# Optimization experiments

Hardware: AMD Instinct MI355X
Metric: run time of the kernel (lower is better)

Reference implementation:

```python
import jax, jax.numpy as jnp
import numpy as np
from jax import lax

T = 32768
DUNITS = 1024
ATT_DIM = 512
EPROJS = 512
ACONV_CHANS = 32
ACONV_FILTS = 15  # kernel = 2*15+1 = 31


def setup_inputs() -> dict:
    key = jax.random.key(0)
    ks = jax.random.split(key, 8)
    dec_z = jax.random.normal(ks[0], (1, DUNITS), jnp.float32)
    att_prev = jax.random.uniform(ks[1], (1, T), jnp.float32)
    att_prev = att_prev / jnp.sum(att_prev, axis=1, keepdims=True)  # prob-like alignment
    pre_compute_enc_h = jax.random.normal(ks[2], (1, T, ATT_DIM), jnp.float32) * 0.1
    enc_h = jax.random.normal(ks[3], (1, T, EPROJS), jnp.float32)
    mask = jnp.zeros((1, T), jnp.float32)  # additive mask (0 = keep)
    conv_w = jax.random.normal(ks[4], (ACONV_CHANS, 1, 2 * ACONV_FILTS + 1), jnp.float32) * 0.1
    conv_b = jnp.zeros((ACONV_CHANS,), jnp.float32)
    W_att = jax.random.normal(ks[5], (ATT_DIM, ACONV_CHANS), jnp.float32) * 0.1
    W_dec = jax.random.normal(ks[6], (ATT_DIM, DUNITS), jnp.float32) * 0.03
    W_g = jax.random.normal(ks[7], (1, ATT_DIM), jnp.float32) * 0.05
    b_g = jnp.zeros((1,), jnp.float32)
    return {"dec_z": dec_z, "att_prev": att_prev, "pre_compute_enc_h": pre_compute_enc_h,
            "enc_h": enc_h, "mask": mask, "conv_w": conv_w, "conv_b": conv_b,
            "W_att": W_att, "W_dec": W_dec, "W_g": W_g, "b_g": b_g}


def reference(dec_z, att_prev, pre_compute_enc_h, enc_h, mask, conv_w, conv_b, W_att, W_dec, W_g, b_g):
    scaling = 2.0
    # location conv: att_prev [1,T] -> [1,C,T] (Conv2d with height-1 kernel == Conv1d)
    att_conv = lax.conv_general_dilated(
        att_prev[:, None, :], conv_w, window_strides=(1,),
        padding=[(ACONV_FILTS, ACONV_FILTS)],
        dimension_numbers=("NCH", "OIH", "NCH"))
    att_conv = att_conv + conv_b[None, :, None]          # [1,C,T]
    att_conv = jnp.einsum("bct,ac->bta", att_conv, W_att)  # mlp_att -> [1,T,att_dim]
    dec_z_tiled = (dec_z @ W_dec.T)[:, None, :]           # [1,1,att_dim]
    # gvec over tanh sum -> energies [1,T]
    e = jnp.einsum("bta,a->bt", jnp.tanh(pre_compute_enc_h + dec_z_tiled + att_conv), W_g[0]) + b_g[0]
    e = e + mask
    w = jax.nn.softmax(scaling * e, axis=1)               # [1,T]
    # forward-attention recurrence: shift-add-mul, then L1 normalize
    att_prev_shift = jnp.pad(att_prev, ((0, 0), (1, 0)))[:, :-1]
    w = (att_prev + att_prev_shift) * w
    w = jnp.clip(w, 1e-6, None)
    w = w / jnp.sum(w, axis=1, keepdims=True)             # L1 normalize (w > 0)
    c = jnp.sum(enc_h * w[:, :, None], axis=1)            # [1,eprojs]
    return (c, w)
```

## Files before the change

### kernel.cpp

```cpp
#include <hip/hip_runtime.h>

#define T_LEN 32768
#define ADIM  512
#define NDEC  1024
#define KTAPS 31

#define WS_BASE 0
#define WS_G    512
#define WS_SARR 16384
#define WS_BMAX 49152
#define WS_BSUM 49664
#define WS_SSUM 50176
#define WS_U    50432
#define WS_CREP 83968

__device__ __forceinline__ float fast_tanh(float x) {
    float e = __expf(2.0f * x);
    return 1.0f - 2.0f * __builtin_amdgcn_rcpf(e + 1.0f);
}

__device__ __forceinline__ float uniform_f(float v) {
    return __uint_as_float(__builtin_amdgcn_readfirstlane(__float_as_uint(v)));
}

__global__ __launch_bounds__(256) void k0_prep(
        const float* __restrict__ dec_z, const float* __restrict__ conv_w,
        const float* __restrict__ conv_b, const float* __restrict__ W_att,
        const float* __restrict__ W_dec, float* __restrict__ ws) {
    int b = blockIdx.x, tid = threadIdx.x;
    int lane = tid & 63, wave = tid >> 6;
    if (b < 64) {
        for (int s = 0; s < 2; ++s) {
            int a = b * 8 + wave * 2 + s;
            float sum = 0.f;
            #pragma unroll
            for (int i = 0; i < 16; ++i)
                sum += W_dec[a * NDEC + i * 64 + lane] * dec_z[i * 64 + lane];
            #pragma unroll
            for (int off = 32; off > 0; off >>= 1) sum += __shfl_xor(sum, off);
            if (lane == 0) {
                float bias = 0.f;
                #pragma unroll
                for (int c = 0; c < 32; ++c) bias += conv_b[c] * W_att[a * 32 + c];
                ws[WS_BASE + a] = sum + bias;
            }
        }
    } else if (b < 64 + KTAPS) {
        int k = b - 64;
        for (int r = 0; r < 2; ++r) {
            int a = tid + r * 256;
            float g = 0.f;
            #pragma unroll
            for (int c = 0; c < 32; ++c) g += conv_w[c * KTAPS + k] * W_att[a * 32 + c];
            ws[WS_G + k * ADIM + a] = g;
        }
    } else {
        if (tid == 0) ws[WS_SSUM] = 0.f;
    }
}

__global__ __launch_bounds__(512, 4) void k1_energy(
        const float* __restrict__ att_prev, const float* __restrict__ pre,
        const float* __restrict__ mask, const float* __restrict__ W_g,
        const float* __restrict__ b_g, float* __restrict__ ws) {
    __shared__ float Gs[KTAPS * ADIM];
    __shared__ float ap_s[96];
    __shared__ float wm[8], wz[8];
    int tid = threadIdx.x, lane = tid & 63, wave = tid >> 6;
    int t0 = blockIdx.x * 64;

    if (blockIdx.x < 32) ws[WS_CREP + blockIdx.x * 512 + tid] = 0.f;

    const float4* Gsrc = (const float4*)(ws + WS_G);
    float4* Gdst = (float4*)Gs;
    #pragma unroll
    for (int i = 0; i < 8; ++i) {
        int idx = tid + i * 512;
        if (idx < 3968) Gdst[idx] = Gsrc[idx];
    }
    if (tid < 94) {
        int g = t0 - 15 + tid;
        ap_s[tid] = (g >= 0 && g < T_LEN) ? att_prev[g] : 0.f;
    }
    __syncthreads();

    float bg = b_g[0];
    int tb_local = wave * 8;
    int tb = t0 + tb_local;

    float ap_u[38];
    #pragma unroll
    for (int i = 0; i < 38; ++i) ap_u[i] = uniform_f(ap_s[tb_local + i]);

    float ps[8];
    #pragma unroll
    for (int j = 0; j < 8; ++j) ps[j] = 0.f;

    #pragma unroll 1
    for (int half = 0; half < 2; ++half) {
        int aa = half * 256 + 4 * lane;
        float4 base = *(const float4*)(ws + WS_BASE + aa);
        float4 wg   = *(const float4*)(W_g + aa);

        float4 p[8];
        #pragma unroll
        for (int j = 0; j < 8; ++j)
            p[j] = *(const float4*)(pre + (size_t)(tb + j) * ADIM + aa);

        float4 acc[8];
        #pragma unroll
        for (int j = 0; j < 8; ++j) acc[j] = base;

        #pragma unroll
        for (int k = 0; k < KTAPS; ++k) {
            float4 g = *(const float4*)(&Gs[k * ADIM + aa]);
            #pragma unroll
            for (int j = 0; j < 8; ++j) {
                float apv = ap_u[j + k];
                acc[j].x = fmaf(apv, g.x, acc[j].x);
                acc[j].y = fmaf(apv, g.y, acc[j].y);
                acc[j].z = fmaf(apv, g.z, acc[j].z);
                acc[j].w = fmaf(apv, g.w, acc[j].w);
            }
        }
        #pragma unroll
        for (int j = 0; j < 8; ++j) {
            float s = ps[j];
            s = fmaf(fast_tanh(p[j].x + acc[j].x), wg.x, s);
            s = fmaf(fast_tanh(p[j].y + acc[j].y), wg.y, s);
            s = fmaf(fast_tanh(p[j].z + acc[j].z), wg.z, s);
            s = fmaf(fast_tanh(p[j].w + acc[j].w), wg.w, s);
            ps[j] = s;
        }
    }

    float m_run = -1e30f, z_run = 0.f;
    #pragma unroll
    for (int j = 0; j < 8; ++j) {
        float e = ps[j];
        #pragma unroll
        for (int off = 32; off > 0; off >>= 1) e += __shfl_xor(e, off);
        int t = tb + j;
        float sv = 2.0f * (e + bg + mask[t]);
        float mn = fmaxf(m_run, sv);
        z_run = z_run * __expf(m_run - mn) + __expf(sv - mn);
        m_run = mn;
        if (lane == 0) ws[WS_SARR + t] = sv;
    }
    if (lane == 0) { wm[wave] = m_run; wz[wave] = z_run; }
    __syncthreads();
    if (tid == 0) {
        float M = wm[0], Z = wz[0];
        #pragma unroll
        for (int w = 1; w < 8; ++w) {
            float mn = fmaxf(M, wm[w]);
            Z = Z * __expf(M - mn) + wz[w] * __expf(wm[w] - mn);
            M = mn;
        }
        ws[WS_BMAX + blockIdx.x] = M;
        ws[WS_BSUM + blockIdx.x] = Z;
    }
}

__global__ __launch_bounds__(512) void k3_context(
        const float* __restrict__ att_prev, const float* __restrict__ enc_h,
        float* __restrict__ ws) {
    __shared__ float wmz[16];
    __shared__ float cbuf[4 * 512];
    int tid = threadIdx.x, lane = tid & 63, wave = tid >> 6;

    float m = ws[WS_BMAX + wave * 64 + lane];
    float z = ws[WS_BSUM + wave * 64 + lane];
    #pragma unroll
    for (int off = 32; off > 0; off >>= 1) {
        float mo = __shfl_xor(m, off), zo = __shfl_xor(z, off);
        float mn = fmaxf(m, mo);
        z = z * __expf(m - mn) + zo * __expf(mo - mn);
        m = mn;
    }
    if (lane == 0) { wmz[wave] = m; wmz[8 + wave] = z; }
    __syncthreads();
    float M = wmz[0], Z = wmz[8];
    #pragma unroll
    for (int w = 1; w < 8; ++w) {
        float mn = fmaxf(M, wmz[w]);
        Z = Z * __expf(M - mn) + wmz[8 + w] * __expf(wmz[w] - mn);
        M = mn;
    }
    float invZ = 1.0f / Z;

    int t0 = blockIdx.x * 32;
    int team = tid >> 7, l = tid & 127;
    int a4 = 4 * l;
    int tbase = t0 + team * 8;
    float4 acc = make_float4(0.f, 0.f, 0.f, 0.f);
    #pragma unroll
    for (int i = 0; i < 8; ++i) {
        int t = tbase + i;
        float ap0 = att_prev[t];
        float apm = (t > 0) ? att_prev[t - 1] : 0.f;
        float u = fmaxf((ap0 + apm) * __expf(ws[WS_SARR + t] - M) * invZ, 1e-6f);
        float4 e = *(const float4*)(enc_h + (size_t)t * ADIM + a4);
        acc.x = fmaf(u, e.x, acc.x);
        acc.y = fmaf(u, e.y, acc.y);
        acc.z = fmaf(u, e.z, acc.z);
        acc.w = fmaf(u, e.w, acc.w);
    }
    if (team != 0) *(float4*)&cbuf[team * 512 + a4] = acc;

    if (tid < 32) {
        int t = t0 + tid;
        float ap0 = att_prev[t];
        float apm = (t > 0) ? att_prev[t - 1] : 0.f;
        float u = fmaxf((ap0 + apm) * __expf(ws[WS_SARR + t] - M) * invZ, 1e-6f);
        ws[WS_U + t] = u;
        float s = u;
        #pragma unroll
        for (int off = 16; off > 0; off >>= 1) s += __shfl_xor(s, off, 32);
        if (tid == 0) atomicAdd(&ws[WS_SSUM], s);
    }
    __syncthreads();
    if (team == 0) {
        float4 b1 = *(const float4*)&cbuf[1 * 512 + a4];
        float4 b2 = *(const float4*)&cbuf[2 * 512 + a4];
        float4 b3 = *(const float4*)&cbuf[3 * 512 + a4];
        float* rep = ws + WS_CREP + (blockIdx.x & 31) * 512;
        atomicAdd(&rep[a4 + 0], acc.x + b1.x + b2.x + b3.x);
        atomicAdd(&rep[a4 + 1], acc.y + b1.y + b2.y + b3.y);
        atomicAdd(&rep[a4 + 2], acc.z + b1.z + b2.z + b3.z);
        atomicAdd(&rep[a4 + 3], acc.w + b1.w + b2.w + b3.w);
    }
}

__global__ __launch_bounds__(512) void k4_final(
        const float* __restrict__ ws, float* __restrict__ out) {
    int b = blockIdx.x, tid = threadIdx.x;
    float invS = 1.0f / ws[WS_SSUM];
    if (b == 0) {
        float acc = 0.f;
        #pragma unroll
        for (int r = 0; r < 32; ++r) acc += ws[WS_CREP + r * 512 + tid];
        out[tid] = acc * invS;
    } else {
        int i = (b - 1) * 512 + tid;
        out[512 + i] = ws[WS_U + i] * invS;
    }
}

extern "C" void kernel_launch(void* const* d_in, const int* in_sizes, int n_in,
                              void* d_out, int out_size, void* d_ws, size_t ws_size,
                              hipStream_t stream) {
    const float* dec_z    = (const float*)d_in[0];
    const float* att_prev = (const float*)d_in[1];
    const float* pre      = (const float*)d_in[2];
    const float* enc_h    = (const float*)d_in[3];
    const float* mask     = (const float*)d_in[4];
    const float* conv_w   = (const float*)d_in[5];
    const float* conv_b   = (const float*)d_in[6];
    const float* W_att    = (const float*)d_in[7];
    const float* W_dec    = (const float*)d_in[8];
    const float* W_g      = (const float*)d_in[9];
    const float* b_g      = (const float*)d_in[10];
    float* out = (float*)d_out;
    float* ws  = (float*)d_ws;

    k0_prep   <<<96,   256, 0, stream>>>(dec_z, conv_w, conv_b, W_att, W_dec, ws);
    k1_energy <<<512,  512, 0, stream>>>(att_prev, pre, mask, W_g, b_g, ws);
    k3_context<<<1024, 512, 0, stream>>>(att_prev, enc_h, ws);
    k4_final  <<<65,   512, 0, stream>>>(ws, out);
}
```

Before: 189.4 us.

## Split attention dim across waves and store conv-folded weights as fp16

The energy kernel now runs 1024 threads per block: each wave handles one half of the attention dimension for 8 time steps, with partial energies combined through shared memory. Previously one wave looped over both halves. The folded conv*W_att weights are precomputed as packed half2 values, which halves the LDS footprint and the bandwidth of the global-to-shared copy. The intent is more parallelism and occupancy and lower register pressure per thread. The costs are an extra block sync and reduced weight precision, which could shift the energies slightly.

```diff
diff --git a/kernel.cpp b/kernel.cpp
--- a/kernel.cpp
+++ b/kernel.cpp
@@ -1,4 +1,5 @@
 #include <hip/hip_runtime.h>
+#include <hip/hip_fp16.h>
 
 #define T_LEN 32768
 #define ADIM  512
@@ -47,36 +48,41 @@
         }
     } else if (b < 64 + KTAPS) {
         int k = b - 64;
-        for (int r = 0; r < 2; ++r) {
-            int a = tid + r * 256;
-            float g = 0.f;
-            #pragma unroll
-            for (int c = 0; c < 32; ++c) g += conv_w[c * KTAPS + k] * W_att[a * 32 + c];
-            ws[WS_G + k * ADIM + a] = g;
-        }
+        int a0 = 2 * tid;
+        float g0 = 0.f, g1 = 0.f;
+        #pragma unroll
+        for (int c = 0; c < 32; ++c) {
+            float w = conv_w[c * KTAPS + k];
+            g0 += w * W_att[a0 * 32 + c];
+            g1 += w * W_att[(a0 + 1) * 32 + c];
+        }
+        __half2 h = __floats2half2_rn(g0, g1);
+        ((unsigned int*)ws)[WS_G + k * 256 + tid] = *(unsigned int*)&h;
     } else {
         if (tid == 0) ws[WS_SSUM] = 0.f;
     }
 }
 
-__global__ __launch_bounds__(512, 4) void k1_energy(
+__global__ __launch_bounds__(1024, 8) void k1_energy(
         const float* __restrict__ att_prev, const float* __restrict__ pre,
         const float* __restrict__ mask, const float* __restrict__ W_g,
         const float* __restrict__ b_g, float* __restrict__ ws) {
-    __shared__ float Gs[KTAPS * ADIM];
+    __shared__ unsigned int Gs[KTAPS * 256];
     __shared__ float ap_s[96];
+    __shared__ float eP[64];
     __shared__ float wm[8], wz[8];
     int tid = threadIdx.x, lane = tid & 63, wave = tid >> 6;
+    int wpair = wave & 7, ah = wave >> 3;
     int t0 = blockIdx.x * 64;
 
-    if (blockIdx.x < 32) ws[WS_CREP + blockIdx.x * 512 + tid] = 0.f;
-
-    const float4* Gsrc = (const float4*)(ws + WS_G);
-    float4* Gdst = (float4*)Gs;
-    #pragma unroll
-    for (int i = 0; i < 8; ++i) {
-        int idx = tid + i * 512;
-        if (idx < 3968) Gdst[idx] = Gsrc[idx];
+    if (blockIdx.x < 16) ws[WS_CREP + blockIdx.x * 1024 + tid] = 0.f;
+
+    const uint4* Gsrc = (const uint4*)((const unsigned int*)ws + WS_G);
+    uint4* Gdst = (uint4*)Gs;
+    #pragma unroll
+    for (int i = 0; i < 2; ++i) {
+        int idx = tid + i * 1024;
+        if (idx < 1984) Gdst[idx] = Gsrc[idx];
     }
     if (tid < 94) {
         int g = t0 - 15 + tid;
@@ -85,69 +91,73 @@
     __syncthreads();
 
     float bg = b_g[0];
-    int tb_local = wave * 8;
+    int tb_local = wpair * 8;
     int tb = t0 + tb_local;
 
     float ap_u[38];
     #pragma unroll
     for (int i = 0; i < 38; ++i) ap_u[i] = uniform_f(ap_s[tb_local + i]);
 
-    float ps[8];
-    #pragma unroll
-    for (int j = 0; j < 8; ++j) ps[j] = 0.f;
-
-    #pragma unroll 1
-    for (int half = 0; half < 2; ++half) {
-        int aa = half * 256 + 4 * lane;
-        float4 base = *(const float4*)(ws + WS_BASE + aa);
-        float4 wg   = *(const float4*)(W_g + aa);
-
-        float4 p[8];
-        #pragma unroll
-        for (int j = 0; j < 8; ++j)
-            p[j] = *(const float4*)(pre + (size_t)(tb + j) * ADIM + aa);
-
-        float4 acc[8];
-        #pragma unroll
-        for (int j = 0; j < 8; ++j) acc[j] = base;
-
-        #pragma unroll
-        for (int k = 0; k < KTAPS; ++k) {
-            float4 g = *(const float4*)(&Gs[k * ADIM + aa]);
-            #pragma unroll
-            for (int j = 0; j < 8; ++j) {
-                float apv = ap_u[j + k];
-                acc[j].x = fmaf(apv, g.x, acc[j].x);
-                acc[j].y = fmaf(apv, g.y, acc[j].y);
-                acc[j].z = fmaf(apv, g.z, acc[j].z);
-                acc[j].w = fmaf(apv, g.w, acc[j].w);
-            }
-        }
+    int aa = ah * 256 + 4 * lane;
+    float4 base = *(const float4*)(ws + WS_BASE + aa);
+
+    float4 acc[8];
+    #pragma unroll
+    for (int j = 0; j < 8; ++j) {
+        float4 p = *(const float4*)(pre + (size_t)(tb + j) * ADIM + aa);
+        acc[j] = make_float4(p.x + base.x, p.y + base.y, p.z + base.z, p.w + base.w);
+    }
+
+    #pragma unroll
+    for (int k = 0; k < KTAPS; ++k) {
+        uint2 g2 = *(const uint2*)&Gs[k * 256 + ah * 128 + 2 * lane];
+        __half2 h0 = *(const __half2*)&g2.x;
+        __half2 h1 = *(const __half2*)&g2.y;
+        float gx = __low2float(h0), gy = __high2float(h0);
+        float gz = __low2float(h1), gw = __high2float(h1);
         #pragma unroll
         for (int j = 0; j < 8; ++j) {
-            float s = ps[j];
-            s = fmaf(fast_tanh(p[j].x + acc[j].x), wg.x, s);
-            s = fmaf(fast_tanh(p[j].y + acc[j].y), wg.y, s);
-            s = fmaf(fast_tanh(p[j].z + acc[j].z), wg.z, s);
-            s = fmaf(fast_tanh(p[j].w + acc[j].w), wg.w, s);
-            ps[j] = s;
-        }
-    }
-
-    float m_run = -1e30f, z_run = 0.f;
+            float apv = ap_u[j + k];
+            acc[j].x = fmaf(apv, gx, acc[j].x);
+            acc[j].y = fmaf(apv, gy, acc[j].y);
+            acc[j].z = fmaf(apv, gz, acc[j].z);
+            acc[j].w = fmaf(apv, gw, acc[j].w);
+        }
+    }
+
+    float4 wg = *(const float4*)(W_g + aa);
+    float e8[8];
     #pragma unroll
     for (int j = 0; j < 8; ++j) {
-        float e = ps[j];
-        #pragma unroll
-        for (int off = 32; off > 0; off >>= 1) e += __shfl_xor(e, off);
-        int t = tb + j;
-        float sv = 2.0f * (e + bg + mask[t]);
-        float mn = fmaxf(m_run, sv);
-        z_run = z_run * __expf(m_run - mn) + __expf(sv - mn);
-        m_run = mn;
-        if (lane == 0) ws[WS_SARR + t] = sv;
-    }
-    if (lane == 0) { wm[wave] = m_run; wz[wave] = z_run; }
+        float s = 0.f;
+        s = fmaf(fast_tanh(acc[j].x), wg.x, s);
+        s = fmaf(fast_tanh(acc[j].y), wg.y, s);
+        s = fmaf(fast_tanh(acc[j].z), wg.z, s);
+        s = fmaf(fast_tanh(acc[j].w), wg.w, s);
+        #pragma unroll
+        for (int off = 32; off > 0; off >>= 1) s += __shfl_xor(s, off);
+        e8[j] = s;
+    }
+
+    if (ah == 1 && lane == 0) {
+        #pragma unroll
+        for (int j = 0; j < 8; ++j) eP[tb_local + j] = e8[j];
+    }
+    __syncthreads();
+
+    if (ah == 0) {
+        float m_run = -1e30f, z_run = 0.f;
+        #pragma unroll
+        for (int j = 0; j < 8; ++j) {
+            int t = tb + j;
+            float sv = 2.0f * (e8[j] + eP[tb_local + j] + bg + mask[t]);
+            float mn = fmaxf(m_run, sv);
+            z_run = z_run * __expf(m_run - mn) + __expf(sv - mn);
+            m_run = mn;
+            if (lane == 0) ws[WS_SARR + t] = sv;
+        }
+        if (lane == 0) { wm[wpair] = m_run; wz[wpair] = z_run; }
+    }
     __syncthreads();
     if (tid == 0) {
         float M = wm[0], Z = wz[0];
@@ -264,8 +274,8 @@
     float* out = (float*)d_out;
     float* ws  = (float*)d_ws;
 
-    k0_prep   <<<96,   256, 0, stream>>>(dec_z, conv_w, conv_b, W_att, W_dec, ws);
-    k1_energy <<<512,  512, 0, stream>>>(att_prev, pre, mask, W_g, b_g, ws);
-    k3_context<<<1024, 512, 0, stream>>>(att_prev, enc_h, ws);
-    k4_final  <<<65,   512, 0, stream>>>(ws, out);
-}
+    k0_prep   <<<96,   256,  0, stream>>>(dec_z, conv_w, conv_b, W_att, W_dec, ws);
+    k1_energy <<<512,  1024, 0, stream>>>(att_prev, pre, mask, W_g, b_g, ws);
+    k3_context<<<1024, 512,  0, stream>>>(att_prev, enc_h, ws);
+    k4_final  <<<65,   512,  0, stream>>>(ws, out);
+}
```

After: 192.5 us. About the same (+1.6%).

## Compute location conv via bf16 MFMA instead of scalar FMA loop

Applied to the files above, without the earlier changes.

Moves the 31-tap convolution times W_att product onto the matrix cores with bf16 16x16x32 MFMA. The folded filter G is stored pre-swizzled in bf16 fragment layout and the att_prev window is built as an A fragment. This drops the large shared-memory copy of G and the per-thread FMA loop. The work is re-split so waves cover time tiles times attention-dim halves, with partial energies combined through shared memory. It adds bf16 rounding error in the conv term and changes the global read pattern for pre (scalar strided loads instead of float4).

```diff
diff --git a/kernel.cpp b/kernel.cpp
--- a/kernel.cpp
+++ b/kernel.cpp
@@ -14,13 +14,17 @@
 #define WS_U    50432
 #define WS_CREP 83968
 
+typedef __attribute__((ext_vector_type(8))) short bf16x8;
+typedef __attribute__((ext_vector_type(4))) float f32x4;
+
 __device__ __forceinline__ float fast_tanh(float x) {
     float e = __expf(2.0f * x);
     return 1.0f - 2.0f * __builtin_amdgcn_rcpf(e + 1.0f);
 }
 
-__device__ __forceinline__ float uniform_f(float v) {
-    return __uint_as_float(__builtin_amdgcn_readfirstlane(__float_as_uint(v)));
+__device__ __forceinline__ unsigned short f2bf(float f) {
+    unsigned u = __float_as_uint(f);
+    return (unsigned short)((u + 0x7FFFu + ((u >> 16) & 1u)) >> 16);
 }
 
 __global__ __launch_bounds__(256) void k0_prep(
@@ -30,6 +34,7 @@
     int b = blockIdx.x, tid = threadIdx.x;
     int lane = tid & 63, wave = tid >> 6;
     if (b < 64) {
+        if (b == 0 && tid == 0) ws[WS_SSUM] = 0.f;
         for (int s = 0; s < 2; ++s) {
             int a = b * 8 + wave * 2 + s;
             float sum = 0.f;
@@ -45,17 +50,21 @@
                 ws[WS_BASE + a] = sum + bias;
             }
         }
-    } else if (b < 64 + KTAPS) {
+    } else {
         int k = b - 64;
-        for (int r = 0; r < 2; ++r) {
-            int a = tid + r * 256;
+        unsigned short* Gf = (unsigned short*)(ws + WS_G);
+        for (int s = 0; s < 2; ++s) {
+            int a = 2 * tid + s;
             float g = 0.f;
-            #pragma unroll
-            for (int c = 0; c < 32; ++c) g += conv_w[c * KTAPS + k] * W_att[a * 32 + c];
-            ws[WS_G + k * ADIM + a] = g;
-        }
-    } else {
-        if (tid == 0) ws[WS_SSUM] = 0.f;
+            if (k < KTAPS) {
+                #pragma unroll
+                for (int c = 0; c < 32; ++c)
+                    g += conv_w[c * KTAPS + k] * W_att[a * 32 + c];
+            }
+            int at = a >> 4, col = a & 15;
+            int l = col | ((k >> 3) << 4), i = k & 7;
+            Gf[(at * 64 + l) * 8 + i] = f2bf(g);
+        }
     }
 }
 
@@ -63,102 +72,74 @@
         const float* __restrict__ att_prev, const float* __restrict__ pre,
         const float* __restrict__ mask, const float* __restrict__ W_g,
         const float* __restrict__ b_g, float* __restrict__ ws) {
-    __shared__ float Gs[KTAPS * ADIM];
     __shared__ float ap_s[96];
-    __shared__ float wm[8], wz[8];
+    __shared__ float eP[2][64];
     int tid = threadIdx.x, lane = tid & 63, wave = tid >> 6;
+    int tt = wave & 3, ah = wave >> 2;
     int t0 = blockIdx.x * 64;
 
     if (blockIdx.x < 32) ws[WS_CREP + blockIdx.x * 512 + tid] = 0.f;
 
-    const float4* Gsrc = (const float4*)(ws + WS_G);
-    float4* Gdst = (float4*)Gs;
-    #pragma unroll
-    for (int i = 0; i < 8; ++i) {
-        int idx = tid + i * 512;
-        if (idx < 3968) Gdst[idx] = Gsrc[idx];
-    }
-    if (tid < 94) {
+    if (tid < 96) {
         int g = t0 - 15 + tid;
         ap_s[tid] = (g >= 0 && g < T_LEN) ? att_prev[g] : 0.f;
     }
     __syncthreads();
 
-    float bg = b_g[0];
-    int tb_local = wave * 8;
-    int tb = t0 + tb_local;
-
-    float ap_u[38];
-    #pragma unroll
-    for (int i = 0; i < 38; ++i) ap_u[i] = uniform_f(ap_s[tb_local + i]);
-
-    float ps[8];
-    #pragma unroll
-    for (int j = 0; j < 8; ++j) ps[j] = 0.f;
-
-    #pragma unroll 1
-    for (int half = 0; half < 2; ++half) {
-        int aa = half * 256 + 4 * lane;
-        float4 base = *(const float4*)(ws + WS_BASE + aa);
-        float4 wg   = *(const float4*)(W_g + aa);
-
-        float4 p[8];
-        #pragma unroll
-        for (int j = 0; j < 8; ++j)
-            p[j] = *(const float4*)(pre + (size_t)(tb + j) * ADIM + aa);
-
-        float4 acc[8];
-        #pragma unroll
-        for (int j = 0; j < 8; ++j) acc[j] = base;
-
-        #pragma unroll
-        for (int k = 0; k < KTAPS; ++k) {
-            float4 g = *(const float4*)(&Gs[k * ADIM + aa]);
-            #pragma unroll
-            for (int j = 0; j < 8; ++j) {
-                float apv = ap_u[j + k];
-                acc[j].x = fmaf(apv, g.x, acc[j].x);
-                acc[j].y = fmaf(apv, g.y, acc[j].y);
-                acc[j].z = fmaf(apv, g.z, acc[j].z);
-                acc[j].w = fmaf(apv, g.w, acc[j].w);
-            }
-        }
-        #pragma unroll
-        for (int j = 0; j < 8; ++j) {
-            float s = ps[j];
-            s = fmaf(fast_tanh(p[j].x + acc[j].x), wg.x, s);
-            s = fmaf(fast_tanh(p[j].y + acc[j].y), wg.y, s);
-            s = fmaf(fast_tanh(p[j].z + acc[j].z), wg.z, s);
-            s = fmaf(fast_tanh(p[j].w + acc[j].w), wg.w, s);
-            ps[j] = s;
-        }
-    }
-
-    float m_run = -1e30f, z_run = 0.f;
-    #pragma unroll
-    for (int j = 0; j < 8; ++j) {
-        float e = ps[j];
-        #pragma unroll
-        for (int off = 32; off > 0; off >>= 1) e += __shfl_xor(e, off);
-        int t = tb + j;
-        float sv = 2.0f * (e + bg + mask[t]);
-        float mn = fmaxf(m_run, sv);
-        z_run = z_run * __expf(m_run - mn) + __expf(sv - mn);
-        m_run = mn;
-        if (lane == 0) ws[WS_SARR + t] = sv;
-    }
-    if (lane == 0) { wm[wave] = m_run; wz[wave] = z_run; }
-    __syncthreads();
-    if (tid == 0) {
-        float M = wm[0], Z = wz[0];
-        #pragma unroll
-        for (int w = 1; w < 8; ++w) {
-            float mn = fmaxf(M, wm[w]);
-            Z = Z * __expf(M - mn) + wz[w] * __expf(wm[w] - mn);
-            M = mn;
-        }
-        ws[WS_BMAX + blockIdx.x] = M;
-        ws[WS_BSUM + blockIdx.x] = Z;
+    int row = lane & 15, g4 = lane >> 4;
+
+    bf16x8 afrag;
+    int aidx = tt * 16 + row + g4 * 8;
+    #pragma unroll
+    for (int i = 0; i < 8; ++i) afrag[i] = (short)f2bf(ap_s[aidx + i]);
+
+    const unsigned short* Gf = (const unsigned short*)(ws + WS_G);
+    float e_acc[4] = {0.f, 0.f, 0.f, 0.f};
+    int tbase = t0 + tt * 16 + g4 * 4;
+
+    #pragma unroll 4
+    for (int p = 0; p < 16; ++p) {
+        int at = ah * 16 + p;
+        int ac = at * 16 + row;
+        bf16x8 bfrag = *(const bf16x8*)(Gf + (size_t)(at * 64 + lane) * 8);
+        float bs = ws[WS_BASE + ac];
+        f32x4 c = {bs, bs, bs, bs};
+        c = __builtin_amdgcn_mfma_f32_16x16x32_bf16(afrag, bfrag, c, 0, 0, 0);
+        float wgv = W_g[ac];
+        #pragma unroll
+        for (int r = 0; r < 4; ++r) {
+            float pv = pre[(size_t)(tbase + r) * ADIM + ac];
+            e_acc[r] = fmaf(fast_tanh(c[r] + pv), wgv, e_acc[r]);
+        }
+    }
+
+    #pragma unroll
+    for (int r = 0; r < 4; ++r) {
+        float s = e_acc[r];
+        s += __shfl_xor(s, 1); s += __shfl_xor(s, 2);
+        s += __shfl_xor(s, 4); s += __shfl_xor(s, 8);
+        e_acc[r] = s;
+    }
+    if (row == 0) {
+        #pragma unroll
+        for (int r = 0; r < 4; ++r) eP[ah][tt * 16 + g4 * 4 + r] = e_acc[r];
+    }
+    __syncthreads();
+
+    if (wave == 0) {
+        int t = t0 + lane;
+        float e = eP[0][lane] + eP[1][lane];
+        float sv = 2.0f * (e + b_g[0] + mask[t]);
+        ws[WS_SARR + t] = sv;
+        float m = sv, z = 1.0f;
+        #pragma unroll
+        for (int off = 32; off > 0; off >>= 1) {
+            float mo = __shfl_xor(m, off), zo = __shfl_xor(z, off);
+            float mn = fmaxf(m, mo);
+            z = z * __expf(m - mn) + zo * __expf(mo - mn);
+            m = mn;
+        }
+        if (lane == 0) { ws[WS_BMAX + blockIdx.x] = m; ws[WS_BSUM + blockIdx.x] = z; }
     }
 }
 
```

New measurement: 186.7 us. About the same (-1.4%).
